# Kernel tuning notes

Measured on AMD Instinct MI355X. Metric: run time of the kernel, lower is better.

The kernel has to match this reference:

```python
import jax, jax.numpy as jnp
import numpy as np

FEATURE_DIM = 128
BATCH = 2
SEQ = 512  # single domain region (0, SEQ) per batch element


def setup_inputs() -> dict:
    key = jax.random.key(0)
    ks = jax.random.split(key, 8)
    D = FEATURE_DIM
    s = lambda fan_in: 1.0 / np.sqrt(fan_in)
    return {
        "domain_features": jax.random.normal(ks[0], (BATCH, SEQ, D), jnp.float32),
        "evolutionary_features": jax.random.normal(ks[1], (BATCH, SEQ, D), jnp.float32),
        # pattern_detector params (jax convention: W is [in, out])
        "W1": jax.random.uniform(ks[2], (2 * D, D), jnp.float32, -s(2 * D), s(2 * D)),
        "b1": jax.random.uniform(ks[3], (D,), jnp.float32, -s(2 * D), s(2 * D)),
        "W2": jax.random.uniform(ks[4], (D, D // 2), jnp.float32, -s(D), s(D)),
        "b2": jax.random.uniform(ks[5], (D // 2,), jnp.float32, -s(D), s(D)),
        "W3": jax.random.uniform(ks[6], (D // 2, 1), jnp.float32, -s(D // 2), s(D // 2)),
        "b3": jax.random.uniform(ks[7], (1,), jnp.float32, -s(D // 2), s(D // 2)),
    }


def reference(domain_features, evolutionary_features, W1, b1, W2, b2, W3, b3):
    D = domain_features.shape[-1]
    # per-position combined feature: g_i = domain_feat[i] * evo_feat[i]
    g = domain_features * evolutionary_features  # [B, N, D]
    # Linear(2D -> D) on cat(g_i, g_j) splits into two halves of W1
    a = jnp.einsum("bnd,de->bne", g, W1[:D])  # contribution of position i
    c = jnp.einsum("bnd,de->bne", g, W1[D:])  # contribution of position j
    h = jax.nn.relu(a[:, :, None, :] + c[:, None, :, :] + b1)       # [B, N, N, D]
    h = jax.nn.relu(jnp.einsum("bijd,de->bije", h, W2) + b2)        # [B, N, N, D//2]
    s = jax.nn.sigmoid(jnp.einsum("bije,e->bij", h, W3[:, 0]) + b3[0])  # [B, N, N]
    # original loop fills only i < j and mirrors; diagonal stays zero
    upper = jnp.triu(s, k=1)
    coevo = upper + jnp.swapaxes(upper, -1, -2)  # symmetric [B, N, N]
    return coevo
```

## Files before the change

### kernel.cpp

```cpp
#include <hip/hip_runtime.h>
#include <hip/hip_bf16.h>

#define D 128
#define Nn 512
#define Bb 2

typedef __bf16 bf16x8_t __attribute__((ext_vector_type(8)));
typedef unsigned short u16x8_t __attribute__((ext_vector_type(8)));
typedef float f32x4_t __attribute__((ext_vector_type(4)));
typedef float f32x8_t __attribute__((ext_vector_type(8)));

__global__ __launch_bounds__(256)
void precompute_ac(const float* __restrict__ dom, const float* __restrict__ evo,
                   const float* __restrict__ W1, const float* __restrict__ b1,
                   const float* __restrict__ W2,
                   float* __restrict__ A, __bf16* __restrict__ Cb,
                   __bf16* __restrict__ W2T) {
    const int t = threadIdx.x;
    const int base = blockIdx.x * 4;
    if (blockIdx.x < 8) {
#pragma unroll
        for (int z = 0; z < 4; ++z) {
            int idx = z * 256 + t;
            int e = blockIdx.x * 8 + (idx >> 7);
            int k = idx & 127;
            W2T[e * 128 + k] = (__bf16)W2[k * 64 + e];
        }
    }
    __shared__ float g4[4][D];
#pragma unroll
    for (int it = 0; it < 2; ++it) {
        int idx = it * 256 + t;
        int r = idx >> 7, c = idx & 127;
        size_t off = (size_t)(base + r) * D + c;
        g4[r][c] = dom[off] * evo[off];
    }
    __syncthreads();
    const int half = t >> 7;
    const int e = t & 127;
    const float* Wp = W1 + half * D * D;
    float a0 = 0.f, a1 = 0.f, a2 = 0.f, a3 = 0.f;
#pragma unroll 8
    for (int dp = 0; dp < D; ++dp) {
        float w = Wp[dp * D + e];
        a0 = fmaf(g4[0][dp], w, a0);
        a1 = fmaf(g4[1][dp], w, a1);
        a2 = fmaf(g4[2][dp], w, a2);
        a3 = fmaf(g4[3][dp], w, a3);
    }
    if (half == 0) {
        float bb = b1[e];
        A[(size_t)(base + 0) * D + e] = a0 + bb;
        A[(size_t)(base + 1) * D + e] = a1 + bb;
        A[(size_t)(base + 2) * D + e] = a2 + bb;
        A[(size_t)(base + 3) * D + e] = a3 + bb;
    } else {
        Cb[(size_t)(base + 0) * D + e] = (__bf16)a0;
        Cb[(size_t)(base + 1) * D + e] = (__bf16)a1;
        Cb[(size_t)(base + 2) * D + e] = (__bf16)a2;
        Cb[(size_t)(base + 3) * D + e] = (__bf16)a3;
    }
}

__global__ __launch_bounds__(256, 4)
void coevo_main(const float* __restrict__ A, const __bf16* __restrict__ Cm,
                const __bf16* __restrict__ W2T, const float* __restrict__ b2,
                const float* __restrict__ W3, const float* __restrict__ b3,
                float* __restrict__ out) {
    const int tid  = threadIdx.x;
    const int wave = tid >> 6;
    const int lane = tid & 63;
    const int m = lane & 15;
    const int q = lane >> 4;

    int u = blockIdx.x;
    const int b = (u >= 576) ? 1 : 0;
    u -= b * 576;
    int chunk = 0;
#pragma unroll
    for (int cc = 1; cc < 8; ++cc) if (u >= 8 * cc * (cc + 1)) chunk = cc;
    const int g = u - 8 * chunk * (chunk + 1);
    const int i = g * 4 + wave;
    const int i0 = g * 4;

    __shared__ __bf16 cs[64 * 128];
    __shared__ __bf16 w2s[64 * 128];
    __shared__ float  tile[4][64];

    const f32x4_t* Cg = (const f32x4_t*)(Cm + ((size_t)b * Nn + (size_t)chunk * 64) * D);
    f32x4_t* csv = (f32x4_t*)cs;
#pragma unroll
    for (int it = 0; it < 4; ++it) {
        int f = it * 256 + tid;
        int r = f >> 4, gi = f & 15;
        csv[r * 16 + (gi ^ (r & 15))] = Cg[f];
    }
    f32x4_t* w2v = (f32x4_t*)w2s;
    const f32x4_t* W2Tg = (const f32x4_t*)W2T;
#pragma unroll
    for (int it = 0; it < 4; ++it) {
        int f = it * 256 + tid;
        int r = f >> 4, gi = f & 15;
        w2v[r * 16 + (gi ^ (r & 15))] = W2Tg[f];
    }

    f32x8_t abv[4];
    {
        const float* Ap = A + ((size_t)(b * Nn + i)) * D + q * 8;
#pragma unroll
        for (int kk = 0; kk < 4; ++kk) {
            f32x4_t v0 = *(const f32x4_t*)(Ap + kk * 32);
            f32x4_t v1 = *(const f32x4_t*)(Ap + kk * 32 + 4);
            f32x8_t v;
            v[0] = v0[0]; v[1] = v0[1]; v[2] = v0[2]; v[3] = v0[3];
            v[4] = v1[0]; v[5] = v1[1]; v[6] = v1[2]; v[7] = v1[3];
            abv[kk] = v;
        }
    }

    float b2v[4], w3v[4];
#pragma unroll
    for (int et = 0; et < 4; ++et) {
        b2v[et] = b2[et * 16 + m];
        w3v[et] = W3[et * 16 + m];
    }
    const float b3s = b3[0];

    __syncthreads();

    const u16x8_t* csr  = (const u16x8_t*)cs;
    const bf16x8_t* w2r = (const bf16x8_t*)w2s;

#pragma unroll
    for (int jt = 0; jt < 4; ++jt) {
        if (chunk * 64 + jt * 16 + 15 < i) continue;
        const int r0  = jt * 16 + m;
        const int key = r0 & 15;

        bf16x8_t af[4];
#pragma unroll
        for (int kk = 0; kk < 4; ++kk) {
            u16x8_t cr = csr[r0 * 16 + ((kk * 4 + q) ^ key)];
            f32x8_t c8;
#pragma unroll
            for (int z = 0; z < 8; ++z)
                c8[z] = __builtin_bit_cast(float, (unsigned)cr[z] << 16);
            f32x8_t t8 = __builtin_elementwise_max(abv[kk] + c8, (f32x8_t)0.f);
            af[kk] = __builtin_convertvector(t8, bf16x8_t);
        }

        float part[4] = {0.f, 0.f, 0.f, 0.f};
#pragma unroll
        for (int et = 0; et < 4; ++et) {
            bf16x8_t wf[4];
#pragma unroll
            for (int kk = 0; kk < 4; ++kk)
                wf[kk] = w2r[(et * 16 + m) * 16 + ((kk * 4 + q) ^ m)];
            f32x4_t a = {0.f, 0.f, 0.f, 0.f};
#pragma unroll
            for (int kk = 0; kk < 4; ++kk)
                a = __builtin_amdgcn_mfma_f32_16x16x32_bf16(af[kk], wf[kk], a, 0, 0, 0);
#pragma unroll
            for (int r = 0; r < 4; ++r)
                part[r] = fmaf(fmaxf(a[r] + b2v[et], 0.f), w3v[et], part[r]);
        }

#pragma unroll
        for (int off = 8; off >= 1; off >>= 1) {
#pragma unroll
            for (int r = 0; r < 4; ++r)
                part[r] += __shfl_xor(part[r], off, 64);
        }
        if (m == 0) {
#pragma unroll
            for (int r = 0; r < 4; ++r) {
                int jc = jt * 16 + q * 4 + r;
                tile[wave][jc] = 1.f / (1.f + expf(-(part[r] + b3s)));
            }
        }
    }

    __syncthreads();

    if ((tid & 63) < 16) {
        const int c4 = tid & 15;
        const int j0 = chunk * 64 + c4 * 4;
        float v0 = tile[wave][c4 * 4 + 0];
        float v1 = tile[wave][c4 * 4 + 1];
        float v2 = tile[wave][c4 * 4 + 2];
        float v3 = tile[wave][c4 * 4 + 3];
        float* op = out + ((size_t)b * Nn + i) * Nn + j0;
        if (j0 > i) {
            f32x4_t v; v[0] = v0; v[1] = v1; v[2] = v2; v[3] = v3;
            *(f32x4_t*)op = v;
        } else if (j0 + 3 >= i) {
            if (j0 + 0 > i) op[0] = v0; else if (j0 + 0 == i) op[0] = 0.f;
            if (j0 + 1 > i) op[1] = v1; else if (j0 + 1 == i) op[1] = 0.f;
            if (j0 + 2 > i) op[2] = v2; else if (j0 + 2 == i) op[2] = 0.f;
            if (j0 + 3 > i) op[3] = v3; else if (j0 + 3 == i) op[3] = 0.f;
        }
    }
    if (tid < 64) {
        const int j = chunk * 64 + tid;
        float v0 = tile[0][tid], v1 = tile[1][tid], v2 = tile[2][tid], v3 = tile[3][tid];
        float* op = out + ((size_t)b * Nn + j) * Nn + i0;
        if (j > i0 + 3) {
            f32x4_t v; v[0] = v0; v[1] = v1; v[2] = v2; v[3] = v3;
            *(f32x4_t*)op = v;
        } else {
            if (j > i0 + 0) op[0] = v0;
            if (j > i0 + 1) op[1] = v1;
            if (j > i0 + 2) op[2] = v2;
            if (j > i0 + 3) op[3] = v3;
        }
    }
}

extern "C" void kernel_launch(void* const* d_in, const int* in_sizes, int n_in,
                              void* d_out, int out_size, void* d_ws, size_t ws_size,
                              hipStream_t stream) {
    const float* dom = (const float*)d_in[0];
    const float* evo = (const float*)d_in[1];
    const float* W1  = (const float*)d_in[2];
    const float* b1  = (const float*)d_in[3];
    const float* W2  = (const float*)d_in[4];
    const float* b2  = (const float*)d_in[5];
    const float* W3  = (const float*)d_in[6];
    const float* b3  = (const float*)d_in[7];
    float* out = (float*)d_out;

    float*  A   = (float*)d_ws;
    __bf16* Cb  = (__bf16*)(A + (size_t)Bb * Nn * D);
    __bf16* W2T = Cb + (size_t)Bb * Nn * D;

    precompute_ac<<<Bb * Nn / 4, 256, 0, stream>>>(dom, evo, W1, b1, W2, A, Cb, W2T);
    coevo_main<<<Bb * 576, 256, 0, stream>>>(A, Cb, W2T, b2, W3, b3, out);
}
```

Baseline: 26.23 us.

## Store A in bf16, read C from global directly, DPP row reduction

Several changes at once. The precompute kernel now handles 2 rows per block instead of 4, doubling its grid, and stores the A projection as bf16 instead of fp32. The main kernel drops the LDS staging of the C chunk and reads C fragments straight from global/L2, which cuts shared memory and lets launch bounds rise from 4 to 5 blocks per CU. It also replaces the shuffle-xor reduction with DPP row reductions. Rounding A to bf16 adds precision loss, and uncoalesced direct global reads of C may cost more than the removed LDS copy.

```diff
diff --git a/kernel.cpp b/kernel.cpp
--- a/kernel.cpp
+++ b/kernel.cpp
@@ -14,10 +14,10 @@
 void precompute_ac(const float* __restrict__ dom, const float* __restrict__ evo,
                    const float* __restrict__ W1, const float* __restrict__ b1,
                    const float* __restrict__ W2,
-                   float* __restrict__ A, __bf16* __restrict__ Cb,
+                   __bf16* __restrict__ A16, __bf16* __restrict__ C16,
                    __bf16* __restrict__ W2T) {
     const int t = threadIdx.x;
-    const int base = blockIdx.x * 4;
+    const int base = blockIdx.x * 2;
     if (blockIdx.x < 8) {
 #pragma unroll
         for (int z = 0; z < 4; ++z) {
@@ -27,43 +27,47 @@
             W2T[e * 128 + k] = (__bf16)W2[k * 64 + e];
         }
     }
-    __shared__ float g4[4][D];
-#pragma unroll
-    for (int it = 0; it < 2; ++it) {
-        int idx = it * 256 + t;
-        int r = idx >> 7, c = idx & 127;
+    __shared__ float g2[2][D];
+    {
+        int r = t >> 7, c = t & 127;
         size_t off = (size_t)(base + r) * D + c;
-        g4[r][c] = dom[off] * evo[off];
+        g2[r][c] = dom[off] * evo[off];
     }
     __syncthreads();
     const int half = t >> 7;
     const int e = t & 127;
     const float* Wp = W1 + half * D * D;
-    float a0 = 0.f, a1 = 0.f, a2 = 0.f, a3 = 0.f;
-#pragma unroll 8
+    float a0 = 0.f, a1 = 0.f;
+#pragma unroll 16
     for (int dp = 0; dp < D; ++dp) {
         float w = Wp[dp * D + e];
-        a0 = fmaf(g4[0][dp], w, a0);
-        a1 = fmaf(g4[1][dp], w, a1);
-        a2 = fmaf(g4[2][dp], w, a2);
-        a3 = fmaf(g4[3][dp], w, a3);
+        a0 = fmaf(g2[0][dp], w, a0);
+        a1 = fmaf(g2[1][dp], w, a1);
     }
     if (half == 0) {
         float bb = b1[e];
-        A[(size_t)(base + 0) * D + e] = a0 + bb;
-        A[(size_t)(base + 1) * D + e] = a1 + bb;
-        A[(size_t)(base + 2) * D + e] = a2 + bb;
-        A[(size_t)(base + 3) * D + e] = a3 + bb;
+        A16[(size_t)(base + 0) * D + e] = (__bf16)(a0 + bb);
+        A16[(size_t)(base + 1) * D + e] = (__bf16)(a1 + bb);
     } else {
-        Cb[(size_t)(base + 0) * D + e] = (__bf16)a0;
-        Cb[(size_t)(base + 1) * D + e] = (__bf16)a1;
-        Cb[(size_t)(base + 2) * D + e] = (__bf16)a2;
-        Cb[(size_t)(base + 3) * D + e] = (__bf16)a3;
-    }
-}
-
-__global__ __launch_bounds__(256, 4)
-void coevo_main(const float* __restrict__ A, const __bf16* __restrict__ Cm,
+        C16[(size_t)(base + 0) * D + e] = (__bf16)a0;
+        C16[(size_t)(base + 1) * D + e] = (__bf16)a1;
+    }
+}
+
+__device__ __forceinline__ float row16_reduce(float x) {
+    int v = __builtin_bit_cast(int, x);
+    x += __builtin_bit_cast(float, __builtin_amdgcn_update_dpp(0, v, 0x118, 0xf, 0xf, false));
+    v = __builtin_bit_cast(int, x);
+    x += __builtin_bit_cast(float, __builtin_amdgcn_update_dpp(0, v, 0x114, 0xf, 0xf, false));
+    v = __builtin_bit_cast(int, x);
+    x += __builtin_bit_cast(float, __builtin_amdgcn_update_dpp(0, v, 0x112, 0xf, 0xf, false));
+    v = __builtin_bit_cast(int, x);
+    x += __builtin_bit_cast(float, __builtin_amdgcn_update_dpp(0, v, 0x111, 0xf, 0xf, false));
+    return x;
+}
+
+__global__ __launch_bounds__(256, 5)
+void coevo_main(const __bf16* __restrict__ A16, const __bf16* __restrict__ Cm,
                 const __bf16* __restrict__ W2T, const float* __restrict__ b2,
                 const float* __restrict__ W3, const float* __restrict__ b3,
                 float* __restrict__ out) {
@@ -83,39 +87,31 @@
     const int i = g * 4 + wave;
     const int i0 = g * 4;
 
-    __shared__ __bf16 cs[64 * 128];
     __shared__ __bf16 w2s[64 * 128];
     __shared__ float  tile[4][64];
 
-    const f32x4_t* Cg = (const f32x4_t*)(Cm + ((size_t)b * Nn + (size_t)chunk * 64) * D);
-    f32x4_t* csv = (f32x4_t*)cs;
-#pragma unroll
-    for (int it = 0; it < 4; ++it) {
-        int f = it * 256 + tid;
-        int r = f >> 4, gi = f & 15;
-        csv[r * 16 + (gi ^ (r & 15))] = Cg[f];
-    }
-    f32x4_t* w2v = (f32x4_t*)w2s;
-    const f32x4_t* W2Tg = (const f32x4_t*)W2T;
-#pragma unroll
-    for (int it = 0; it < 4; ++it) {
-        int f = it * 256 + tid;
-        int r = f >> 4, gi = f & 15;
-        w2v[r * 16 + (gi ^ (r & 15))] = W2Tg[f];
+    const u16x8_t* Ag8 = (const u16x8_t*)(A16 + ((size_t)(b * Nn + i)) * D);
+    u16x8_t ab16[4];
+#pragma unroll
+    for (int kk = 0; kk < 4; ++kk) ab16[kk] = Ag8[kk * 4 + q];
+
+    {
+        f32x4_t* w2v = (f32x4_t*)w2s;
+        const f32x4_t* W2Tg = (const f32x4_t*)W2T;
+#pragma unroll
+        for (int it = 0; it < 4; ++it) {
+            int f = it * 256 + tid;
+            int r = f >> 4, gi = f & 15;
+            w2v[r * 16 + (gi ^ (r & 15))] = W2Tg[f];
+        }
     }
 
     f32x8_t abv[4];
-    {
-        const float* Ap = A + ((size_t)(b * Nn + i)) * D + q * 8;
-#pragma unroll
-        for (int kk = 0; kk < 4; ++kk) {
-            f32x4_t v0 = *(const f32x4_t*)(Ap + kk * 32);
-            f32x4_t v1 = *(const f32x4_t*)(Ap + kk * 32 + 4);
-            f32x8_t v;
-            v[0] = v0[0]; v[1] = v0[1]; v[2] = v0[2]; v[3] = v0[3];
-            v[4] = v1[0]; v[5] = v1[1]; v[6] = v1[2]; v[7] = v1[3];
-            abv[kk] = v;
-        }
+#pragma unroll
+    for (int kk = 0; kk < 4; ++kk) {
+#pragma unroll
+        for (int z = 0; z < 8; ++z)
+            abv[kk][z] = __builtin_bit_cast(float, (unsigned)ab16[kk][z] << 16);
     }
 
     float b2v[4], w3v[4];
@@ -128,19 +124,18 @@
 
     __syncthreads();
 
-    const u16x8_t* csr  = (const u16x8_t*)cs;
+    const u16x8_t*  Cg8 = (const u16x8_t*)(Cm + ((size_t)b * Nn + (size_t)chunk * 64) * D);
     const bf16x8_t* w2r = (const bf16x8_t*)w2s;
 
 #pragma unroll
     for (int jt = 0; jt < 4; ++jt) {
         if (chunk * 64 + jt * 16 + 15 < i) continue;
-        const int r0  = jt * 16 + m;
-        const int key = r0 & 15;
+        const int r0 = jt * 16 + m;
 
         bf16x8_t af[4];
 #pragma unroll
         for (int kk = 0; kk < 4; ++kk) {
-            u16x8_t cr = csr[r0 * 16 + ((kk * 4 + q) ^ key)];
+            u16x8_t cr = Cg8[r0 * 16 + kk * 4 + q];
             f32x8_t c8;
 #pragma unroll
             for (int z = 0; z < 8; ++z)
@@ -165,17 +160,14 @@
                 part[r] = fmaf(fmaxf(a[r] + b2v[et], 0.f), w3v[et], part[r]);
         }
 
-#pragma unroll
-        for (int off = 8; off >= 1; off >>= 1) {
-#pragma unroll
-            for (int r = 0; r < 4; ++r)
-                part[r] += __shfl_xor(part[r], off, 64);
-        }
-        if (m == 0) {
+        float red[4];
+#pragma unroll
+        for (int r = 0; r < 4; ++r) red[r] = row16_reduce(part[r]);
+        if (m == 15) {
 #pragma unroll
             for (int r = 0; r < 4; ++r) {
                 int jc = jt * 16 + q * 4 + r;
-                tile[wave][jc] = 1.f / (1.f + expf(-(part[r] + b3s)));
+                tile[wave][jc] = 1.f / (1.f + expf(-(red[r] + b3s)));
             }
         }
     }
@@ -229,10 +221,10 @@
     const float* b3  = (const float*)d_in[7];
     float* out = (float*)d_out;
 
-    float*  A   = (float*)d_ws;
-    __bf16* Cb  = (__bf16*)(A + (size_t)Bb * Nn * D);
-    __bf16* W2T = Cb + (size_t)Bb * Nn * D;
-
-    precompute_ac<<<Bb * Nn / 4, 256, 0, stream>>>(dom, evo, W1, b1, W2, A, Cb, W2T);
-    coevo_main<<<Bb * 576, 256, 0, stream>>>(A, Cb, W2T, b2, W3, b3, out);
-}
+    __bf16* A16 = (__bf16*)d_ws;
+    __bf16* C16 = A16 + (size_t)Bb * Nn * D;
+    __bf16* W2T = C16 + (size_t)Bb * Nn * D;
+
+    precompute_ac<<<Bb * Nn / 2, 256, 0, stream>>>(dom, evo, W1, b1, W2, A16, C16, W2T);
+    coevo_main<<<Bb * 576, 256, 0, stream>>>(A16, C16, W2T, b2, W3, b3, out);
+}
```

Measured after the change: 25.68 us, median of 2. 1.02x faster.
